# Kernel tuning notes

Hardware: AMD Instinct MI355X
Metric: run time of the kernel (lower is better)

Reference implementation:

```python
import jax, jax.numpy as jnp
import numpy as np

N_ATOMS = 1_000_000
DESC_DIM = 128
HIDDEN = 128
N_ELEM = 4  # element ids 0..3


def setup_inputs() -> dict:
    key = jax.random.key(0)
    ks = jax.random.split(key, 6)
    element = jax.random.randint(ks[0], (N_ATOMS,), 0, N_ELEM, dtype=jnp.int32)
    desc = jax.random.normal(ks[1], (N_ATOMS, DESC_DIM), dtype=jnp.float32)
    # Per-element MLP experts: desc_dim -> hidden -> 1
    W1 = jax.random.normal(ks[2], (N_ELEM, DESC_DIM, HIDDEN), dtype=jnp.float32) / np.sqrt(DESC_DIM)
    b1 = jnp.zeros((N_ELEM, HIDDEN), dtype=jnp.float32)
    W2 = jax.random.normal(ks[3], (N_ELEM, HIDDEN), dtype=jnp.float32) / np.sqrt(HIDDEN)
    b2 = jnp.zeros((N_ELEM,), dtype=jnp.float32)
    return {"element": element, "desc": desc, "W1": W1, "b1": b1, "W2": W2, "b2": b2}


def reference(element, desc, W1, b1, W2, b2):
    """Per-element dispatch: each atom's descriptor goes through the MLP for
    its atomic number. JAX jit needs static shapes, so we compute each
    expert densely and select with where (loop over small fixed expert set)."""
    out = jnp.zeros(desc.shape[0], dtype=desc.dtype)
    for e in range(W1.shape[0]):
        h = jax.nn.relu(desc @ W1[e] + b1[e])      # [N, HIDDEN]
        y = h @ W2[e] + b2[e]                       # [N]
        out = jnp.where(element == e, y, out)
    return out
```

## Files before the change

### kernel.cpp

```cpp
#include <hip/hip_runtime.h>
#include <hip/hip_bf16.h>

typedef __attribute__((ext_vector_type(8))) short short8;
typedef __attribute__((ext_vector_type(4))) float float4v;

__device__ __forceinline__ unsigned short f2bf(float f) {
    unsigned int u = __float_as_uint(f);
    u += 0x7fffu + ((u >> 16) & 1u);
    return (unsigned short)(u >> 16);
}

__global__ void count_kernel(const int* __restrict__ elem, int n, int* __restrict__ bc) {
    const int t = threadIdx.x, b = blockIdx.x;
    const int base = b * 1024;
    int c[4] = {0, 0, 0, 0};
    #pragma unroll
    for (int i = 0; i < 4; ++i) {
        const int a = base + i * 256 + t;
        if (a < n) c[elem[a]]++;
    }
    int p0 = c[0] | (c[1] << 16);
    int p1 = c[2] | (c[3] << 16);
    #pragma unroll
    for (int off = 1; off < 64; off <<= 1) { p0 += __shfl_xor(p0, off); p1 += __shfl_xor(p1, off); }
    __shared__ int wsum[4][4];
    const int w = t >> 6, lane = t & 63;
    if (lane == 0) {
        wsum[w][0] = p0 & 0xffff; wsum[w][1] = p0 >> 16;
        wsum[w][2] = p1 & 0xffff; wsum[w][3] = p1 >> 16;
    }
    __syncthreads();
    if (t < 4) {
        int s = 0;
        #pragma unroll
        for (int ww = 0; ww < 4; ++ww) s += wsum[ww][t];
        bc[b * 4 + t] = s;
    }
}

__global__ void scan_kernel(int* __restrict__ bc, int* __restrict__ offs, int nb) {
    const int t = threadIdx.x, w = t >> 6, lane = t & 63;
    int vals[16];
    int s = 0;
    #pragma unroll
    for (int j = 0; j < 16; ++j) {
        const int i = lane * 16 + j;
        const int v = (i < nb) ? bc[i * 4 + w] : 0;
        vals[j] = s; s += v;
    }
    int incl = s;
    #pragma unroll
    for (int off = 1; off < 64; off <<= 1) {
        const int v = __shfl_up(incl, off);
        if (lane >= off) incl += v;
    }
    const int excl = incl - s;
    __shared__ int tot[4];
    __shared__ int eoff[4];
    if (lane == 63) tot[w] = incl;
    __syncthreads();
    if (t == 0) {
        int a = 0;
        for (int e = 0; e < 4; ++e) { eoff[e] = a; offs[e] = a; a += tot[e]; }
        offs[4] = a;
    }
    __syncthreads();
    const int myoff = eoff[w] + excl;
    #pragma unroll
    for (int j = 0; j < 16; ++j) {
        const int i = lane * 16 + j;
        if (i < nb) bc[i * 4 + w] = myoff + vals[j];
    }
}

__global__ void scatter_kernel(const int* __restrict__ elem, int n,
                               const int* __restrict__ bc, int* __restrict__ idx_sorted) {
    const int t = threadIdx.x, b = blockIdx.x;
    const int w = t >> 6, lane = t & 63;
    const int base = b * 1024;
    int ev[4];
    #pragma unroll
    for (int i = 0; i < 4; ++i) {
        const int a = base + i * 256 + t;
        ev[i] = (a < n) ? elem[a] : -1;
    }
    __shared__ int tbl[4][4][4];
    __shared__ int sbase[4];
    #pragma unroll
    for (int i = 0; i < 4; ++i) {
        #pragma unroll
        for (int el = 0; el < 4; ++el) {
            const unsigned long long m = __ballot(ev[i] == el);
            if (lane == 0) tbl[i][w][el] = (int)__popcll(m);
        }
    }
    if (t < 4) sbase[t] = bc[b * 4 + t];
    __syncthreads();
    if (t < 4) {
        int s = 0;
        for (int i = 0; i < 4; ++i)
            for (int w2 = 0; w2 < 4; ++w2) { const int v = tbl[i][w2][t]; tbl[i][w2][t] = s; s += v; }
    }
    __syncthreads();
    #pragma unroll
    for (int i = 0; i < 4; ++i) {
        unsigned long long m[4];
        #pragma unroll
        for (int el = 0; el < 4; ++el) m[el] = __ballot(ev[i] == el);
        const int a = base + i * 256 + t;
        if (a < n) {
            const int el = ev[i];
            const int rank = (int)__popcll(m[el] & ((1ull << lane) - 1ull));
            idx_sorted[sbase[el] + tbl[i][w][el] + rank] = a;
        }
    }
}

__global__ void w1t_kernel(const float* __restrict__ W1, unsigned short* __restrict__ W1T) {
    const int b = blockIdx.x;
    const int e = b >> 7, nn = b & 127;
    const int k = threadIdx.x;
    const float v = W1[((size_t)(e * 128 + k)) * 128 + nn];
    W1T[((size_t)(e * 128 + nn)) * 128 + k] = f2bf(v);
}

__global__ __launch_bounds__(256, 2)
void expert_mlp_kernel(const float* __restrict__ desc,
                       const unsigned short* __restrict__ W1T,
                       const float* __restrict__ b1,
                       const float* __restrict__ W2,
                       const float* __restrict__ b2,
                       const int* __restrict__ idx_sorted,
                       const int* __restrict__ offs,
                       float* __restrict__ out) {
    __shared__ unsigned short As[128 * 128];
    __shared__ unsigned short Bs[128 * 128];

    const int bx = blockIdx.x;
    const int e = bx & 3;
    const int tile = bx >> 2;
    const int base = offs[e];
    const int cnt = offs[e + 1] - base;
    const int m0 = tile * 128;
    if (m0 >= cnt) return;
    const int t = threadIdx.x;

    {
        const uint4* src = (const uint4*)(W1T + (size_t)e * 16384);
        const int c = t & 15, nrow = t >> 4;
        #pragma unroll
        for (int p = 0; p < 8; ++p) {
            const int nn = nrow + p * 16;
            const uint4 v = src[nn * 16 + c];
            const int pc = c ^ (nn & 7);
            *(uint4*)(&Bs[nn * 128 + pc * 8]) = v;
        }
    }
    {
        const int c = t & 31, rr = t >> 5;
        #pragma unroll
        for (int p = 0; p < 16; ++p) {
            const int r = p * 8 + rr;
            const int gm = m0 + r;
            const int gi = idx_sorted[base + ((gm < cnt) ? gm : 0)];
            const float4 v = *(const float4*)(desc + (size_t)gi * 128 + c * 4);
            ushort4 pk;
            pk.x = f2bf(v.x); pk.y = f2bf(v.y); pk.z = f2bf(v.z); pk.w = f2bf(v.w);
            const int pc = (c >> 1) ^ (r & 7);
            *(ushort4*)(&As[r * 128 + pc * 8 + (c & 1) * 4]) = pk;
        }
    }
    __syncthreads();

    const int lane = t & 63;
    const int wv = t >> 6;
    const int quad = lane >> 4;
    const int l16 = lane & 15;
    const int mbase = wv * 32;
    const int r7 = l16 & 7;

    float4v acc[2][8] = {};
    #pragma unroll
    for (int ks = 0; ks < 4; ++ks) {
        const int pco = ((ks * 4 + quad) ^ r7) * 8;
        const short8 a0 = *(const short8*)(&As[(mbase + l16) * 128 + pco]);
        const short8 a1 = *(const short8*)(&As[(mbase + 16 + l16) * 128 + pco]);
        #pragma unroll
        for (int nt = 0; nt < 8; ++nt) {
            const short8 bf = *(const short8*)(&Bs[(nt * 16 + l16) * 128 + pco]);
            acc[0][nt] = __builtin_amdgcn_mfma_f32_16x16x32_bf16(a0, bf, acc[0][nt], 0, 0, 0);
            acc[1][nt] = __builtin_amdgcn_mfma_f32_16x16x32_bf16(a1, bf, acc[1][nt], 0, 0, 0);
        }
    }

    float b1v[8], w2v[8];
    #pragma unroll
    for (int nt = 0; nt < 8; ++nt) {
        b1v[nt] = b1[e * 128 + nt * 16 + l16];
        w2v[nt] = W2[e * 128 + nt * 16 + l16];
    }
    const float b2e = b2[e];
    #pragma unroll
    for (int mt = 0; mt < 2; ++mt) {
        float y[4] = {0.f, 0.f, 0.f, 0.f};
        #pragma unroll
        for (int nt = 0; nt < 8; ++nt) {
            const float4v v = acc[mt][nt];
            #pragma unroll
            for (int r = 0; r < 4; ++r)
                y[r] += fmaxf(v[r] + b1v[nt], 0.f) * w2v[nt];
        }
        #pragma unroll
        for (int off = 1; off < 16; off <<= 1) {
            #pragma unroll
            for (int r = 0; r < 4; ++r) y[r] += __shfl_xor(y[r], off, 16);
        }
        if (l16 == 0) {
            #pragma unroll
            for (int r = 0; r < 4; ++r) {
                const int m = mbase + mt * 16 + quad * 4 + r;
                const int gm = m0 + m;
                if (gm < cnt) out[idx_sorted[base + gm]] = y[r] + b2e;
            }
        }
    }
}

extern "C" void kernel_launch(void* const* d_in, const int* in_sizes, int n_in,
                              void* d_out, int out_size, void* d_ws, size_t ws_size,
                              hipStream_t stream) {
    const int*   elem = (const int*)d_in[0];
    const float* desc = (const float*)d_in[1];
    const float* W1   = (const float*)d_in[2];
    const float* b1   = (const float*)d_in[3];
    const float* W2   = (const float*)d_in[4];
    const float* b2   = (const float*)d_in[5];
    float* out = (float*)d_out;
    const int n = in_sizes[0];

    char* ws = (char*)d_ws;
    int* bc         = (int*)ws;
    int* offs       = (int*)(ws + 16128);
    int* idx_sorted = (int*)(ws + 16384);
    unsigned short* W1T = (unsigned short*)(ws + 16384 + (size_t)n * 4);

    const int nb = (n + 1023) / 1024;
    count_kernel  <<<nb, 256, 0, stream>>>(elem, n, bc);
    scan_kernel   <<<1, 256, 0, stream>>>(bc, offs, nb);
    scatter_kernel<<<nb, 256, 0, stream>>>(elem, n, bc, idx_sorted);
    w1t_kernel    <<<512, 128, 0, stream>>>(W1, W1T);

    const int tiles = (n + 127) / 128;
    expert_mlp_kernel<<<tiles * 4, 256, 0, stream>>>(desc, W1T, b1, W2, b2, idx_sorted, offs, out);
}
```

Baseline: 692.2 us.

## Replace sort-and-dispatch pipeline with fused persistent dense-expert kernel

Drops the count, scan, scatter and weight-transpose kernels and launches one persistent kernel that evaluates all four experts densely on each 32-row tile, keeping only the result for each atom's own element. W1 is converted to bf16 into registers once per block, and descriptor tiles are double-buffered in shared memory with register prefetch. This removes the sorting passes, the indirect gathers and the extra launches, but does four times the MFMA work. It also runs only 256 blocks with a large register footprint, so occupancy may be low.

```diff
diff --git a/kernel.cpp b/kernel.cpp
--- a/kernel.cpp
+++ b/kernel.cpp
@@ -1,5 +1,4 @@
 #include <hip/hip_runtime.h>
-#include <hip/hip_bf16.h>
 
 typedef __attribute__((ext_vector_type(8))) short short8;
 typedef __attribute__((ext_vector_type(4))) float float4v;
@@ -10,189 +9,47 @@
     return (unsigned short)(u >> 16);
 }
 
-__global__ void count_kernel(const int* __restrict__ elem, int n, int* __restrict__ bc) {
-    const int t = threadIdx.x, b = blockIdx.x;
-    const int base = b * 1024;
-    int c[4] = {0, 0, 0, 0};
-    #pragma unroll
-    for (int i = 0; i < 4; ++i) {
-        const int a = base + i * 256 + t;
-        if (a < n) c[elem[a]]++;
-    }
-    int p0 = c[0] | (c[1] << 16);
-    int p1 = c[2] | (c[3] << 16);
-    #pragma unroll
-    for (int off = 1; off < 64; off <<= 1) { p0 += __shfl_xor(p0, off); p1 += __shfl_xor(p1, off); }
-    __shared__ int wsum[4][4];
-    const int w = t >> 6, lane = t & 63;
-    if (lane == 0) {
-        wsum[w][0] = p0 & 0xffff; wsum[w][1] = p0 >> 16;
-        wsum[w][2] = p1 & 0xffff; wsum[w][3] = p1 >> 16;
-    }
-    __syncthreads();
-    if (t < 4) {
-        int s = 0;
+#define GRID 256
+#define MT   32
+
+__global__ __launch_bounds__(512, 2)
+void fused_moe_kernel(const int* __restrict__ elem,
+                      const float* __restrict__ desc,
+                      const float* __restrict__ W1,
+                      const float* __restrict__ b1,
+                      const float* __restrict__ W2,
+                      const float* __restrict__ b2,
+                      float* __restrict__ out, int n) {
+    __shared__ unsigned short As[2][MT * 128];
+
+    const int ntiles = (n + MT - 1) / MT;
+    int tile = blockIdx.x;
+    if (tile >= ntiles) return;
+
+    const int t    = threadIdx.x;
+    const int wv   = t >> 6;
+    const int lane = t & 63;
+    const int quad = lane >> 4;
+    const int l16  = lane & 15;
+    const int e    = wv & 3;
+    const int mb   = (wv >> 2) * 16;
+    const int r7   = l16 & 7;
+
+    short8 bfr[4][8];
+    {
+        const float* Wp = W1 + (size_t)e * 16384 + (size_t)(quad * 8) * 128 + l16;
         #pragma unroll
-        for (int ww = 0; ww < 4; ++ww) s += wsum[ww][t];
-        bc[b * 4 + t] = s;
-    }
-}
-
-__global__ void scan_kernel(int* __restrict__ bc, int* __restrict__ offs, int nb) {
-    const int t = threadIdx.x, w = t >> 6, lane = t & 63;
-    int vals[16];
-    int s = 0;
-    #pragma unroll
-    for (int j = 0; j < 16; ++j) {
-        const int i = lane * 16 + j;
-        const int v = (i < nb) ? bc[i * 4 + w] : 0;
-        vals[j] = s; s += v;
-    }
-    int incl = s;
-    #pragma unroll
-    for (int off = 1; off < 64; off <<= 1) {
-        const int v = __shfl_up(incl, off);
-        if (lane >= off) incl += v;
-    }
-    const int excl = incl - s;
-    __shared__ int tot[4];
-    __shared__ int eoff[4];
-    if (lane == 63) tot[w] = incl;
-    __syncthreads();
-    if (t == 0) {
-        int a = 0;
-        for (int e = 0; e < 4; ++e) { eoff[e] = a; offs[e] = a; a += tot[e]; }
-        offs[4] = a;
-    }
-    __syncthreads();
-    const int myoff = eoff[w] + excl;
-    #pragma unroll
-    for (int j = 0; j < 16; ++j) {
-        const int i = lane * 16 + j;
-        if (i < nb) bc[i * 4 + w] = myoff + vals[j];
-    }
-}
-
-__global__ void scatter_kernel(const int* __restrict__ elem, int n,
-                               const int* __restrict__ bc, int* __restrict__ idx_sorted) {
-    const int t = threadIdx.x, b = blockIdx.x;
-    const int w = t >> 6, lane = t & 63;
-    const int base = b * 1024;
-    int ev[4];
-    #pragma unroll
-    for (int i = 0; i < 4; ++i) {
-        const int a = base + i * 256 + t;
-        ev[i] = (a < n) ? elem[a] : -1;
-    }
-    __shared__ int tbl[4][4][4];
-    __shared__ int sbase[4];
-    #pragma unroll
-    for (int i = 0; i < 4; ++i) {
-        #pragma unroll
-        for (int el = 0; el < 4; ++el) {
-            const unsigned long long m = __ballot(ev[i] == el);
-            if (lane == 0) tbl[i][w][el] = (int)__popcll(m);
+        for (int ks = 0; ks < 4; ++ks) {
+            #pragma unroll
+            for (int nt = 0; nt < 8; ++nt) {
+                const float* p = Wp + (size_t)(ks * 32) * 128 + nt * 16;
+                short8 b;
+                #pragma unroll
+                for (int j = 0; j < 8; ++j) b[j] = (short)f2bf(p[(size_t)j * 128]);
+                bfr[ks][nt] = b;
+            }
         }
     }
-    if (t < 4) sbase[t] = bc[b * 4 + t];
-    __syncthreads();
-    if (t < 4) {
-        int s = 0;
-        for (int i = 0; i < 4; ++i)
-            for (int w2 = 0; w2 < 4; ++w2) { const int v = tbl[i][w2][t]; tbl[i][w2][t] = s; s += v; }
-    }
-    __syncthreads();
-    #pragma unroll
-    for (int i = 0; i < 4; ++i) {
-        unsigned long long m[4];
-        #pragma unroll
-        for (int el = 0; el < 4; ++el) m[el] = __ballot(ev[i] == el);
-        const int a = base + i * 256 + t;
-        if (a < n) {
-            const int el = ev[i];
-            const int rank = (int)__popcll(m[el] & ((1ull << lane) - 1ull));
-            idx_sorted[sbase[el] + tbl[i][w][el] + rank] = a;
-        }
-    }
-}
-
-__global__ void w1t_kernel(const float* __restrict__ W1, unsigned short* __restrict__ W1T) {
-    const int b = blockIdx.x;
-    const int e = b >> 7, nn = b & 127;
-    const int k = threadIdx.x;
-    const float v = W1[((size_t)(e * 128 + k)) * 128 + nn];
-    W1T[((size_t)(e * 128 + nn)) * 128 + k] = f2bf(v);
-}
-
-__global__ __launch_bounds__(256, 2)
-void expert_mlp_kernel(const float* __restrict__ desc,
-                       const unsigned short* __restrict__ W1T,
-                       const float* __restrict__ b1,
-                       const float* __restrict__ W2,
-                       const float* __restrict__ b2,
-                       const int* __restrict__ idx_sorted,
-                       const int* __restrict__ offs,
-                       float* __restrict__ out) {
-    __shared__ unsigned short As[128 * 128];
-    __shared__ unsigned short Bs[128 * 128];
-
-    const int bx = blockIdx.x;
-    const int e = bx & 3;
-    const int tile = bx >> 2;
-    const int base = offs[e];
-    const int cnt = offs[e + 1] - base;
-    const int m0 = tile * 128;
-    if (m0 >= cnt) return;
-    const int t = threadIdx.x;
-
-    {
-        const uint4* src = (const uint4*)(W1T + (size_t)e * 16384);
-        const int c = t & 15, nrow = t >> 4;
-        #pragma unroll
-        for (int p = 0; p < 8; ++p) {
-            const int nn = nrow + p * 16;
-            const uint4 v = src[nn * 16 + c];
-            const int pc = c ^ (nn & 7);
-            *(uint4*)(&Bs[nn * 128 + pc * 8]) = v;
-        }
-    }
-    {
-        const int c = t & 31, rr = t >> 5;
-        #pragma unroll
-        for (int p = 0; p < 16; ++p) {
-            const int r = p * 8 + rr;
-            const int gm = m0 + r;
-            const int gi = idx_sorted[base + ((gm < cnt) ? gm : 0)];
-            const float4 v = *(const float4*)(desc + (size_t)gi * 128 + c * 4);
-            ushort4 pk;
-            pk.x = f2bf(v.x); pk.y = f2bf(v.y); pk.z = f2bf(v.z); pk.w = f2bf(v.w);
-            const int pc = (c >> 1) ^ (r & 7);
-            *(ushort4*)(&As[r * 128 + pc * 8 + (c & 1) * 4]) = pk;
-        }
-    }
-    __syncthreads();
-
-    const int lane = t & 63;
-    const int wv = t >> 6;
-    const int quad = lane >> 4;
-    const int l16 = lane & 15;
-    const int mbase = wv * 32;
-    const int r7 = l16 & 7;
-
-    float4v acc[2][8] = {};
-    #pragma unroll
-    for (int ks = 0; ks < 4; ++ks) {
-        const int pco = ((ks * 4 + quad) ^ r7) * 8;
-        const short8 a0 = *(const short8*)(&As[(mbase + l16) * 128 + pco]);
-        const short8 a1 = *(const short8*)(&As[(mbase + 16 + l16) * 128 + pco]);
-        #pragma unroll
-        for (int nt = 0; nt < 8; ++nt) {
-            const short8 bf = *(const short8*)(&Bs[(nt * 16 + l16) * 128 + pco]);
-            acc[0][nt] = __builtin_amdgcn_mfma_f32_16x16x32_bf16(a0, bf, acc[0][nt], 0, 0, 0);
-            acc[1][nt] = __builtin_amdgcn_mfma_f32_16x16x32_bf16(a1, bf, acc[1][nt], 0, 0, 0);
-        }
-    }
-
     float b1v[8], w2v[8];
     #pragma unroll
     for (int nt = 0; nt < 8; ++nt) {
@@ -200,29 +57,85 @@
         w2v[nt] = W2[e * 128 + nt * 16 + l16];
     }
     const float b2e = b2[e];
+
+    const int c  = t & 31;
+    const int r0 = (t >> 5) * 2;
+
+    float4 rv[2];
     #pragma unroll
-    for (int mt = 0; mt < 2; ++mt) {
+    for (int p = 0; p < 2; ++p) {
+        int rg = tile * MT + r0 + p;
+        if (rg >= n) rg = n - 1;
+        rv[p] = *(const float4*)(desc + (size_t)rg * 128 + c * 4);
+    }
+    #pragma unroll
+    for (int p = 0; p < 2; ++p) {
+        const int r = r0 + p;
+        ushort4 pk;
+        pk.x = f2bf(rv[p].x); pk.y = f2bf(rv[p].y);
+        pk.z = f2bf(rv[p].z); pk.w = f2bf(rv[p].w);
+        const int pc = (c >> 1) ^ (r & 7);
+        *(ushort4*)(&As[0][r * 128 + pc * 8 + (c & 1) * 4]) = pk;
+    }
+    __syncthreads();
+
+    int buf = 0;
+    for (; tile < ntiles; tile += GRID) {
+        const int nxt = tile + GRID;
+        const bool has_next = (nxt < ntiles);
+        if (has_next) {
+            #pragma unroll
+            for (int p = 0; p < 2; ++p) {
+                int rg = nxt * MT + r0 + p;
+                if (rg >= n) rg = n - 1;
+                rv[p] = *(const float4*)(desc + (size_t)rg * 128 + c * 4);
+            }
+        }
+
+        float4v acc[8] = {};
+        #pragma unroll
+        for (int ks = 0; ks < 4; ++ks) {
+            const int pco = ((ks * 4 + quad) ^ r7) * 8;
+            const short8 a0 = *(const short8*)(&As[buf][(mb + l16) * 128 + pco]);
+            #pragma unroll
+            for (int nt = 0; nt < 8; ++nt)
+                acc[nt] = __builtin_amdgcn_mfma_f32_16x16x32_bf16(a0, bfr[ks][nt], acc[nt], 0, 0, 0);
+        }
+
         float y[4] = {0.f, 0.f, 0.f, 0.f};
         #pragma unroll
         for (int nt = 0; nt < 8; ++nt) {
-            const float4v v = acc[mt][nt];
+            const float4v v = acc[nt];
             #pragma unroll
-            for (int r = 0; r < 4; ++r)
-                y[r] += fmaxf(v[r] + b1v[nt], 0.f) * w2v[nt];
+            for (int rr = 0; rr < 4; ++rr)
+                y[rr] += fmaxf(v[rr] + b1v[nt], 0.f) * w2v[nt];
         }
         #pragma unroll
         for (int off = 1; off < 16; off <<= 1) {
             #pragma unroll
-            for (int r = 0; r < 4; ++r) y[r] += __shfl_xor(y[r], off, 16);
+            for (int rr = 0; rr < 4; ++rr) y[rr] += __shfl_xor(y[rr], off, 16);
         }
         if (l16 == 0) {
             #pragma unroll
-            for (int r = 0; r < 4; ++r) {
-                const int m = mbase + mt * 16 + quad * 4 + r;
-                const int gm = m0 + m;
-                if (gm < cnt) out[idx_sorted[base + gm]] = y[r] + b2e;
+            for (int rr = 0; rr < 4; ++rr) {
+                const int gm = tile * MT + mb + quad * 4 + rr;
+                if (gm < n && elem[gm] == e) out[gm] = y[rr] + b2e;
             }
         }
+
+        if (has_next) {
+            #pragma unroll
+            for (int p = 0; p < 2; ++p) {
+                const int r = r0 + p;
+                ushort4 pk;
+                pk.x = f2bf(rv[p].x); pk.y = f2bf(rv[p].y);
+                pk.z = f2bf(rv[p].z); pk.w = f2bf(rv[p].w);
+                const int pc = (c >> 1) ^ (r & 7);
+                *(ushort4*)(&As[buf ^ 1][r * 128 + pc * 8 + (c & 1) * 4]) = pk;
+            }
+        }
+        __syncthreads();
+        buf ^= 1;
     }
 }
 
@@ -237,19 +150,7 @@
     const float* b2   = (const float*)d_in[5];
     float* out = (float*)d_out;
     const int n = in_sizes[0];
+    if (n <= 0) return;
 
-    char* ws = (char*)d_ws;
-    int* bc         = (int*)ws;
-    int* offs       = (int*)(ws + 16128);
-    int* idx_sorted = (int*)(ws + 16384);
-    unsigned short* W1T = (unsigned short*)(ws + 16384 + (size_t)n * 4);
-
-    const int nb = (n + 1023) / 1024;
-    count_kernel  <<<nb, 256, 0, stream>>>(elem, n, bc);
-    scan_kernel   <<<1, 256, 0, stream>>>(bc, offs, nb);
-    scatter_kernel<<<nb, 256, 0, stream>>>(elem, n, bc, idx_sorted);
-    w1t_kernel    <<<512, 128, 0, stream>>>(W1, W1T);
-
-    const int tiles = (n + 127) / 128;
-    expert_mlp_kernel<<<tiles * 4, 256, 0, stream>>>(desc, W1T, b1, W2, b2, idx_sorted, offs, out);
+    fused_moe_kernel<<<GRID, 512, 0, stream>>>(elem, desc, W1, b1, W2, b2, out, n);
 }
```

Result: slower. 768.3 us (+11.0%).
